# Kernel tuning notes

Hardware: AMD Instinct MI355X
Metric: run time of the kernel (lower is better)

Reference implementation:

```python
import jax, jax.numpy as jnp
import numpy as np

B, S, LQ = 32, 1024, 128
EMB = 256; H = 256; NH = 8; DH = H // NH
NCATE, NCONT, NNODE = 4, 8, 4
VOCAB = 50000
EPS = 1e-5
LK = S - LQ


def _ln(x, g, b):
    mu = jnp.mean(x, -1, keepdims=True)
    xc = x - mu
    var = jnp.mean(xc * xc, -1, keepdims=True)
    return xc * jax.lax.rsqrt(var + EPS) * g + b


def _leaky(x):
    return jnp.where(x >= 0, x, 0.01 * x)  # LeakyReLU slope 0.01 (torch default)


def setup_inputs() -> dict:
    key = jax.random.key(0)
    ks = jax.random.split(key, 48)
    rnd = lambda i, shape, scale=0.02: jax.random.normal(ks[i], shape, dtype=jnp.float32) * scale
    rng = np.random.default_rng(0)
    qidx = jnp.asarray(np.sort(rng.choice(S, LQ, replace=False)).astype(np.int64))
    cate_table = rnd(6, (VOCAB, EMB)).at[0].set(0.0)  # padding_idx=0
    inp = {
        "node": jax.random.normal(ks[0], (B, S, EMB * NNODE), dtype=jnp.float32),
        "cate": jax.random.randint(ks[1], (B, S, NCATE), 0, VOCAB),
        "cont": jax.random.normal(ks[2], (B, S, NCONT), dtype=jnp.float32),
        "query_index": qidx,
        "mask": jax.random.bernoulli(ks[3], 0.1, (B, LK)),
        "cate_table": cate_table,
        "pos_emb": rnd(4, (1, S, H)),
        "node_W": rnd(5, (EMB * NNODE, H)), "node_b": jnp.zeros((H,), jnp.float32),
        "node_ln_g": jnp.ones((H,), jnp.float32), "node_ln_b": jnp.zeros((H,), jnp.float32),
        "cate_W": rnd(7, (EMB * NCATE, H)), "cate_b": jnp.zeros((H,), jnp.float32),
        "cate_ln_g": jnp.ones((H,), jnp.float32), "cate_ln_b": jnp.zeros((H,), jnp.float32),
        "bn_g": jnp.ones((NCONT,), jnp.float32), "bn_b": jnp.zeros((NCONT,), jnp.float32),
        "cont_W": rnd(8, (NCONT, H)), "cont_b": jnp.zeros((H,), jnp.float32),
        "cont_ln_g": jnp.ones((H,), jnp.float32), "cont_ln_b": jnp.zeros((H,), jnp.float32),
        "comb_W": rnd(9, (3 * H, H)), "comb_b": jnp.zeros((H,), jnp.float32),
        "comb_ln_g": jnp.ones((H,), jnp.float32), "comb_ln_b": jnp.zeros((H,), jnp.float32),
        "q_W": rnd(10, (H, H)), "q_b": jnp.zeros((H,), jnp.float32),
        "k_W": rnd(11, (H, H)), "k_b": jnp.zeros((H,), jnp.float32),
        "v_W": rnd(12, (H, H)), "v_b": jnp.zeros((H,), jnp.float32),
        "reg_W1": rnd(13, (H, H)), "reg_b1": jnp.zeros((H,), jnp.float32),
        "reg_ln_g": jnp.ones((H,), jnp.float32), "reg_ln_b": jnp.zeros((H,), jnp.float32),
        "reg_W2": rnd(14, (H, H)), "reg_b2": jnp.zeros((H,), jnp.float32),
    }
    return inp


def reference(node, cate, cont, query_index, mask, cate_table, pos_emb,
              node_W, node_b, node_ln_g, node_ln_b,
              cate_W, cate_b, cate_ln_g, cate_ln_b,
              bn_g, bn_b, cont_W, cont_b, cont_ln_g, cont_ln_b,
              comb_W, comb_b, comb_ln_g, comb_ln_b,
              q_W, q_b, k_W, k_b, v_W, v_b,
              reg_W1, reg_b1, reg_ln_g, reg_ln_b, reg_W2, reg_b2):
    # --- three embedding branches: Linear -> LayerNorm ---
    node_e = _ln(node @ node_W + node_b, node_ln_g, node_ln_b)
    ce = cate_table[cate].reshape(B, S, NCATE * EMB)  # embedding gather
    cate_e = _ln(ce @ cate_W + cate_b, cate_ln_g, cate_ln_b)
    # BatchNorm1d (training-mode batch stats, biased var) over flattened [B*S, C]
    cf = cont.reshape(-1, NCONT)
    mu = jnp.mean(cf, 0)
    var = jnp.mean((cf - mu) ** 2, 0)
    cn = ((cf - mu) * jax.lax.rsqrt(var + EPS) * bn_g + bn_b).reshape(B, S, NCONT)
    cont_e = _ln(cn @ cont_W + cont_b, cont_ln_g, cont_ln_b)
    # --- combine + positions ---
    seq = jnp.concatenate([node_e, cate_e, cont_e], -1)       # [B,S,3H]
    seq = _ln(_leaky(seq) @ comb_W + comb_b, comb_ln_g, comb_ln_b) + pos_emb  # [B,S,H]
    # --- gather-split cross attention: queries vs complement keys ---
    is_q = jnp.zeros((S,), bool).at[query_index].set(True)
    key_index = jnp.nonzero(~is_q, size=LK)[0]                # setdiff1d, static size
    q = seq[:, query_index]                                   # [B,LQ,H]
    kv = seq[:, key_index]                                    # [B,LK,H]
    Q = (q @ q_W + q_b).reshape(B, LQ, NH, DH).transpose(0, 2, 1, 3)
    K = (kv @ k_W + k_b).reshape(B, LK, NH, DH).transpose(0, 2, 1, 3)
    V = (kv @ v_W + v_b).reshape(B, LK, NH, DH).transpose(0, 2, 1, 3)
    scale = jnp.float32(1.0 / np.sqrt(DH))
    scores = jnp.einsum('bhqd,bhkd->bhqk', Q, K) * scale      # [B,NH,LQ,LK]
    scores = jnp.where(mask[:, None, None, :], jnp.float32(-1e9), scores)
    attn = jax.nn.softmax(scores, -1)                         # dropout = identity (eval)
    out = jnp.einsum('bhqk,bhkd->bhqd', attn, V).transpose(0, 2, 1, 3).reshape(B, LQ, H)
    h = _leaky(_ln(out @ reg_W1 + reg_b1, reg_ln_g, reg_ln_b))
    return h @ reg_W2 + reg_b2                                # [B,LQ,H]
```

## Files before the change

kernel.cpp:

```cpp
#include <hip/hip_runtime.h>
#include <cstdint>

#define EPSV 1e-5f
#define AS1 __attribute__((address_space(1)))
#define AS3 __attribute__((address_space(3)))

#define VMCNT_BAR(N) do { \
    asm volatile("s_waitcnt vmcnt(" #N ") lgkmcnt(0)" ::: "memory"); \
    __builtin_amdgcn_sched_barrier(0); \
    __builtin_amdgcn_s_barrier(); } while (0)

typedef __attribute__((ext_vector_type(8))) short short8v;
typedef __attribute__((ext_vector_type(4))) float float4v;

__device__ inline unsigned short f2bf(float f) {
    union { float f; unsigned int u; } v; v.f = f;
    unsigned int r = v.u + 0x7FFF + ((v.u >> 16) & 1);
    return (unsigned short)(r >> 16);
}

__device__ inline size_t bidx(int n, int k) {
    return ((size_t)(k >> 5) << 13) + ((size_t)(n >> 4) << 9)
         + (((k >> 3) & 3) << 7) + ((n & 15) << 3) + (k & 7);
}

__device__ inline void gld16(const unsigned short* g, unsigned short* d) {
    __builtin_amdgcn_global_load_lds((const AS1 void*)g, (AS3 void*)d, 16, 0, 0);
}

__device__ inline void issue_b(const unsigned short* Bc, int s, unsigned short* bsb,
                               int w, int l) {
    const unsigned short* g = Bc + ((size_t)s << 13) + (w << 9) + (l << 3);
    unsigned short* d = bsb + (w << 9) + (l << 3);
    #pragma unroll
    for (int i = 0; i < 4; ++i)
        gld16(g + (i << 11), d + (i << 11));
}

__global__ __launch_bounds__(256) void wt_all_k(
    const float* __restrict__ nW, const float* __restrict__ cW, const float* __restrict__ mW,
    const float* __restrict__ qW, const float* __restrict__ kW, const float* __restrict__ vW,
    const float* __restrict__ r1W, const float* __restrict__ r2W,
    unsigned short* __restrict__ nO, unsigned short* __restrict__ cO, unsigned short* __restrict__ mO,
    unsigned short* __restrict__ qO, unsigned short* __restrict__ kO, unsigned short* __restrict__ vO,
    unsigned short* __restrict__ r1O, unsigned short* __restrict__ r2O)
{
    __shared__ float T[64][65];
    int bid = blockIdx.x;
    const float* W; unsigned short* O; int K, tile;
    if (bid < 64)       { W = nW; O = nO; K = 1024; tile = bid; }
    else if (bid < 128) { W = cW; O = cO; K = 1024; tile = bid - 64; }
    else if (bid < 176) { W = mW; O = mO; K = 768;  tile = bid - 128; }
    else {
        int s = (bid - 176) >> 4; tile = (bid - 176) & 15; K = 256;
        switch (s) {
            case 0: W = qW;  O = qO;  break;
            case 1: W = kW;  O = kO;  break;
            case 2: W = vW;  O = vO;  break;
            case 3: W = r1W; O = r1O; break;
            default: W = r2W; O = r2O; break;
        }
    }
    int kTiles = K >> 6;
    int k0 = (tile % kTiles) * 64, n0 = (tile / kTiles) * 64;
    int c = threadIdx.x & 63, r4 = threadIdx.x >> 6;
    #pragma unroll
    for (int rr = 0; rr < 64; rr += 4) {
        int r = rr + r4;
        T[r][c] = W[(size_t)(k0 + r) * 256 + n0 + c];
    }
    __syncthreads();
    #pragma unroll
    for (int rr = 0; rr < 64; rr += 4) {
        int n = rr + r4;
        O[bidx(n0 + n, k0 + c)] = f2bf(T[c][n]);
    }
}

__global__ __launch_bounds__(256) void gemm_nc_k(
    const float* __restrict__ node, const int* __restrict__ cate,
    const float* __restrict__ table,
    const unsigned short* __restrict__ nWt, const unsigned short* __restrict__ cWt,
    const float* __restrict__ nb, const float* __restrict__ cb,
    const float* __restrict__ nlg, const float* __restrict__ nlb,
    const float* __restrict__ clg, const float* __restrict__ clb,
    unsigned short* __restrict__ Y)
{
    __shared__ union UN {
        unsigned short A[2][4096];
        struct { float S[64][4]; float Q[64][4]; } red;
    } U;
    __shared__ unsigned short Bs[2][16384];
    const int t = threadIdx.x;
    const bool isC = blockIdx.x >= 512;
    const int bm = (isC ? (int)blockIdx.x - 512 : (int)blockIdx.x) * 64;
    const int w = t >> 6, l = t & 63, lr = l & 15, lg = l >> 4;
    const int ar = t >> 2;
    const int ac = (t & 3) * 16;
    const int aw0 = (((t & 3) >> 1) << 11) + ((ar >> 4) << 9)
                  + ((((t & 3) * 2) & 3) << 7) + ((ar & 15) << 3);
    const int aw1 = aw0 + 128;

    const unsigned short* Bc = isC ? cWt : nWt;
    const float* bias = isC ? cb : nb;
    const float* lng  = isC ? clg : nlg;
    const float* lnbp = isC ? clb : nlb;
    const int colOff = isC ? 256 : 0;

    const float* apf = node + (size_t)(bm + ar) * 1024 + ac;
    int4 idx4 = {0,0,0,0};
    if (isC) idx4 = *(const int4*)&cate[(bm + ar) * 4];

    float4v acc[4][4];
    #pragma unroll
    for (int i = 0; i < 4; ++i)
        #pragma unroll
        for (int j = 0; j < 4; ++j) acc[i][j] = (float4v)0.f;

    float4 rA[4];

    auto loadA = [&](int s, float4 (&r)[4]) {
        const float* p;
        if (isC) {
            int kt = s * 64 + ac;
            int g = kt >> 8;
            int idx = (g == 0) ? idx4.x : (g == 1) ? idx4.y : (g == 2) ? idx4.z : idx4.w;
            p = table + (size_t)idx * 256 + (kt & 255);
        } else {
            p = apf + s * 64;
        }
        #pragma unroll
        for (int i = 0; i < 4; ++i) r[i] = *(const float4*)(p + i * 4);
    };
    auto writeA = [&](const float4 (&r)[4], unsigned short* Ab) {
        short8v v0, v1;
        v0[0] = (short)f2bf(r[0].x); v0[1] = (short)f2bf(r[0].y);
        v0[2] = (short)f2bf(r[0].z); v0[3] = (short)f2bf(r[0].w);
        v0[4] = (short)f2bf(r[1].x); v0[5] = (short)f2bf(r[1].y);
        v0[6] = (short)f2bf(r[1].z); v0[7] = (short)f2bf(r[1].w);
        v1[0] = (short)f2bf(r[2].x); v1[1] = (short)f2bf(r[2].y);
        v1[2] = (short)f2bf(r[2].z); v1[3] = (short)f2bf(r[2].w);
        v1[4] = (short)f2bf(r[3].x); v1[5] = (short)f2bf(r[3].y);
        v1[6] = (short)f2bf(r[3].z); v1[7] = (short)f2bf(r[3].w);
        *(short8v*)&Ab[aw0] = v0;
        *(short8v*)&Ab[aw1] = v1;
    };
    auto comp = [&](const unsigned short* Ab, const unsigned short* bsb) {
        #pragma unroll
        for (int kk = 0; kk < 2; ++kk) {
            short8v af[4], bf[4];
            #pragma unroll
            for (int i = 0; i < 4; ++i)
                af[i] = *(const short8v*)&Ab[kk*2048 + i*512 + lg*128 + lr*8];
            #pragma unroll
            for (int j = 0; j < 4; ++j)
                bf[j] = *(const short8v*)&bsb[kk*8192 + ((w*4 + j) << 9) + (lg << 7) + (lr << 3)];
            #pragma unroll
            for (int i = 0; i < 4; ++i)
                #pragma unroll
                for (int j = 0; j < 4; ++j)
                    acc[i][j] = __builtin_amdgcn_mfma_f32_16x16x32_bf16(af[i], bf[j], acc[i][j], 0, 0, 0);
        }
    };

    issue_b(Bc, 0, &Bs[0][0], w, l);
    issue_b(Bc, 1, &Bs[0][8192], w, l);
    loadA(0, rA);
    writeA(rA, U.A[0]);
    loadA(1, rA);
    asm volatile("s_waitcnt lgkmcnt(0)" ::: "memory");
    __builtin_amdgcn_sched_barrier(0);
    __builtin_amdgcn_s_barrier();

    for (int s = 0; s < 16; ++s) {
        const int cur = s & 1;
        if (s + 1 < 16) {
            issue_b(Bc, 2*(s+1),     &Bs[1 - cur][0],    w, l);
            issue_b(Bc, 2*(s+1) + 1, &Bs[1 - cur][8192], w, l);
        }
        comp(U.A[cur], &Bs[cur][0]);
        if (s + 1 < 16) {
            writeA(rA, U.A[1 - cur]);
            if (s + 2 < 16) {
                loadA(s + 2, rA);
                VMCNT_BAR(4);
            } else {
                VMCNT_BAR(0);
            }
        }
    }

    #pragma unroll
    for (int j = 0; j < 4; ++j) {
        float bvj = bias[w*64 + j*16 + lr];
        #pragma unroll
        for (int i = 0; i < 4; ++i)
            #pragma unroll
            for (int r4 = 0; r4 < 4; ++r4) acc[i][j][r4] += bvj;
    }
    __syncthreads();
    #pragma unroll
    for (int i = 0; i < 4; ++i) {
        float ps[4], qs[4];
        #pragma unroll
        for (int r4 = 0; r4 < 4; ++r4) {
            float a0 = acc[i][0][r4], a1 = acc[i][1][r4],
                  a2 = acc[i][2][r4], a3 = acc[i][3][r4];
            ps[r4] = (a0 + a1) + (a2 + a3);
            qs[r4] = (a0*a0 + a1*a1) + (a2*a2 + a3*a3);
        }
        #pragma unroll
        for (int o = 1; o < 16; o <<= 1)
            #pragma unroll
            for (int r4 = 0; r4 < 4; ++r4) {
                ps[r4] += __shfl_xor(ps[r4], o);
                qs[r4] += __shfl_xor(qs[r4], o);
            }
        if (lr == 0) {
            #pragma unroll
            for (int r4 = 0; r4 < 4; ++r4) {
                U.red.S[i*16 + lg*4 + r4][w] = ps[r4];
                U.red.Q[i*16 + lg*4 + r4][w] = qs[r4];
            }
        }
    }
    __syncthreads();
    #pragma unroll
    for (int i = 0; i < 4; ++i) {
        float mu[4], rstd[4];
        #pragma unroll
        for (int r4 = 0; r4 < 4; ++r4) {
            int rl = i*16 + lg*4 + r4;
            float s  = (U.red.S[rl][0] + U.red.S[rl][1]) + (U.red.S[rl][2] + U.red.S[rl][3]);
            float qq = (U.red.Q[rl][0] + U.red.Q[rl][1]) + (U.red.Q[rl][2] + U.red.Q[rl][3]);
            float m_ = s * (1.0f/256.0f);
            mu[r4] = m_;
            rstd[r4] = rsqrtf(qq * (1.0f/256.0f) - m_*m_ + EPSV);
        }
        #pragma unroll
        for (int j = 0; j < 4; ++j) {
            int c = w*64 + j*16 + lr;
            float gv = lng[c], b2 = lnbp[c];
            #pragma unroll
            for (int r4 = 0; r4 < 4; ++r4) {
                int row = bm + i*16 + lg*4 + r4;
                float y = (acc[i][j][r4] - mu[r4]) * rstd[r4] * gv + b2;
                y = (y >= 0.f) ? y : 0.01f*y;
                Y[(size_t)row * 768 + colOff + c] = f2bf(y);
            }
        }
    }
}

__global__ __launch_bounds__(256) void gemm_comb_k(
    const unsigned short* __restrict__ A,
    const unsigned short* __restrict__ Bc,
    const float* __restrict__ bias,
    const float* __restrict__ lng, const float* __restrict__ lnbp,
    const float* __restrict__ pos,
    unsigned short* __restrict__ Y)
{
    __shared__ union UC {
        unsigned short A[2][2048];
        struct { float S[32][4]; float Q[32][4]; } red;
    } U;
    __shared__ unsigned short Bs[2][16384];
    const int t = threadIdx.x;
    const int bm = blockIdx.x * 32;
    const int w = t >> 6, l = t & 63, lr = l & 15, lg = l >> 4;
    const int arow = t >> 3;
    const int ake  = (t & 7) * 8;
    const int awo = (((t & 7) >> 2) << 10) + ((arow >> 4) << 9)
                  + (((t & 7) & 3) << 7) + ((arow & 15) << 3);

    const unsigned short* ap = A + (size_t)(bm + arow) * 768 + ake;

    float4v acc[2][4];
    #pragma unroll
    for (int i = 0; i < 2; ++i)
        #pragma unroll
        for (int j = 0; j < 4; ++j) acc[i][j] = (float4v)0.f;

    short8v aA;

    auto comp = [&](const unsigned short* Ab, const unsigned short* bsb) {
        #pragma unroll
        for (int kk = 0; kk < 2; ++kk) {
            short8v af[2], bf[4];
            #pragma unroll
            for (int i = 0; i < 2; ++i)
                af[i] = *(const short8v*)&Ab[kk*1024 + i*512 + lg*128 + lr*8];
            #pragma unroll
            for (int j = 0; j < 4; ++j)
                bf[j] = *(const short8v*)&bsb[kk*8192 + ((w*4 + j) << 9) + (lg << 7) + (lr << 3)];
            #pragma unroll
            for (int i = 0; i < 2; ++i)
                #pragma unroll
                for (int j = 0; j < 4; ++j)
                    acc[i][j] = __builtin_amdgcn_mfma_f32_16x16x32_bf16(af[i], bf[j], acc[i][j], 0, 0, 0);
        }
    };

    issue_b(Bc, 0, &Bs[0][0], w, l);
    issue_b(Bc, 1, &Bs[0][8192], w, l);
    aA = *(const short8v*)(ap);
    *(short8v*)&U.A[0][awo] = aA;
    aA = *(const short8v*)(ap + 64);
    asm volatile("s_waitcnt lgkmcnt(0)" ::: "memory");
    __builtin_amdgcn_sched_barrier(0);
    __builtin_amdgcn_s_barrier();

    for (int s = 0; s < 12; ++s) {
        const int cur = s & 1;
        if (s + 1 < 12) {
            issue_b(Bc, 2*(s+1),     &Bs[1 - cur][0],    w, l);
            issue_b(Bc, 2*(s+1) + 1, &Bs[1 - cur][8192], w, l);
        }
        comp(U.A[cur], &Bs[cur][0]);
        if (s + 1 < 12) {
            *(short8v*)&U.A[1 - cur][awo] = aA;
            if (s + 2 < 12) {
                aA = *(const short8v*)(ap + (s + 2) * 64);
                VMCNT_BAR(1);
            } else {
                VMCNT_BAR(0);
            }
        }
    }

    #pragma unroll
    for (int j = 0; j < 4; ++j) {
        float bvj = bias[w*64 + j*16 + lr];
        #pragma unroll
        for (int i = 0; i < 2; ++i)
            #pragma unroll
            for (int r4 = 0; r4 < 4; ++r4) acc[i][j][r4] += bvj;
    }
    __syncthreads();
    #pragma unroll
    for (int i = 0; i < 2; ++i) {
        float ps[4], qs[4];
        #pragma unroll
        for (int r4 = 0; r4 < 4; ++r4) {
            float a0 = acc[i][0][r4], a1 = acc[i][1][r4],
                  a2 = acc[i][2][r4], a3 = acc[i][3][r4];
            ps[r4] = (a0 + a1) + (a2 + a3);
            qs[r4] = (a0*a0 + a1*a1) + (a2*a2 + a3*a3);
        }
        #pragma unroll
        for (int o = 1; o < 16; o <<= 1)
            #pragma unroll
            for (int r4 = 0; r4 < 4; ++r4) {
                ps[r4] += __shfl_xor(ps[r4], o);
                qs[r4] += __shfl_xor(qs[r4], o);
            }
        if (lr == 0) {
            #pragma unroll
            for (int r4 = 0; r4 < 4; ++r4) {
                U.red.S[i*16 + lg*4 + r4][w] = ps[r4];
                U.red.Q[i*16 + lg*4 + r4][w] = qs[r4];
            }
        }
    }
    __syncthreads();
    #pragma unroll
    for (int i = 0; i < 2; ++i) {
        float mu[4], rstd[4];
        #pragma unroll
        for (int r4 = 0; r4 < 4; ++r4) {
            int rl = i*16 + lg*4 + r4;
            float s  = (U.red.S[rl][0] + U.red.S[rl][1]) + (U.red.S[rl][2] + U.red.S[rl][3]);
            float qq = (U.red.Q[rl][0] + U.red.Q[rl][1]) + (U.red.Q[rl][2] + U.red.Q[rl][3]);
            float m_ = s * (1.0f/256.0f);
            mu[r4] = m_;
            rstd[r4] = rsqrtf(qq * (1.0f/256.0f) - m_*m_ + EPSV);
        }
        #pragma unroll
        for (int j = 0; j < 4; ++j) {
            int c = w*64 + j*16 + lr;
            float gv = lng[c], b2 = lnbp[c];
            #pragma unroll
            for (int r4 = 0; r4 < 4; ++r4) {
                int row = bm + i*16 + lg*4 + r4;
                float y = (acc[i][j][r4] - mu[r4]) * rstd[r4] * gv + b2
                        + pos[(size_t)(row & 1023) * 256 + c];
                Y[(size_t)row * 256 + c] = f2bf(y);
            }
        }
    }
}

__global__ __launch_bounds__(256) void gemm_qkv_k(
    const unsigned short* __restrict__ seq,
    const int* __restrict__ qmap, const int* __restrict__ krmap,
    const unsigned short* __restrict__ qWt, const unsigned short* __restrict__ kWt,
    const unsigned short* __restrict__ vWt,
    const float* __restrict__ qb, const float* __restrict__ kb, const float* __restrict__ vb,
    unsigned short* __restrict__ Qo, unsigned short* __restrict__ Ko,
    unsigned short* __restrict__ Vt)
{
    __shared__ unsigned short Asl[2][4096];
    __shared__ unsigned short Bs[2][16384];
    const int t = threadIdx.x;
    const int bid = blockIdx.x;
    int seg, bm;
    const int* gmap; const unsigned short* Bc; const float* bias;
    if (bid < 64)       { seg = 0; bm = bid * 64;         gmap = qmap;  Bc = qWt; bias = qb; }
    else if (bid < 512) { seg = 1; bm = (bid - 64) * 64;  gmap = krmap; Bc = kWt; bias = kb; }
    else                { seg = 2; bm = (bid - 512) * 64; gmap = krmap; Bc = vWt; bias = vb; }
    const int w = t >> 6, l = t & 63, lr = l & 15, lg = l >> 4;
    const int ar = t >> 2;
    const int ac = (t & 3) * 16;
    const int aw0 = (((t & 3) >> 1) << 11) + ((ar >> 4) << 9)
                  + ((((t & 3) * 2) & 3) << 7) + ((ar & 15) << 3);
    const int aw1 = aw0 + 128;

    const unsigned short* ap = seq + (size_t)gmap[bm + ar] * 256 + ac;

    float4v acc[4][4];
    #pragma unroll
    for (int i = 0; i < 4; ++i)
        #pragma unroll
        for (int j = 0; j < 4; ++j) acc[i][j] = (float4v)0.f;

    short8v a0A, a1A;

    auto comp = [&](const unsigned short* Ab, const unsigned short* bsb) {
        #pragma unroll
        for (int kk = 0; kk < 2; ++kk) {
            short8v af[4], bf[4];
            #pragma unroll
            for (int i = 0; i < 4; ++i)
                af[i] = *(const short8v*)&Ab[kk*2048 + i*512 + lg*128 + lr*8];
            #pragma unroll
            for (int j = 0; j < 4; ++j)
                bf[j] = *(const short8v*)&bsb[kk*8192 + ((w*4 + j) << 9) + (lg << 7) + (lr << 3)];
            #pragma unroll
            for (int i = 0; i < 4; ++i)
                #pragma unroll
                for (int j = 0; j < 4; ++j)
                    acc[i][j] = __builtin_amdgcn_mfma_f32_16x16x32_bf16(af[i], bf[j], acc[i][j], 0, 0, 0);
        }
    };

    issue_b(Bc, 0, &Bs[0][0], w, l);
    issue_b(Bc, 1, &Bs[0][8192], w, l);
    a0A = *(const short8v*)(ap);
    a1A = *(const short8v*)(ap + 8);
    *(short8v*)&Asl[0][aw0] = a0A;
    *(short8v*)&Asl[0][aw1] = a1A;
    a0A = *(const short8v*)(ap + 64);
    a1A = *(const short8v*)(ap + 72);
    asm volatile("s_waitcnt lgkmcnt(0)" ::: "memory");
    __builtin_amdgcn_sched_barrier(0);
    __builtin_amdgcn_s_barrier();

    for (int s = 0; s < 4; ++s) {
        const int cur = s & 1;
        if (s + 1 < 4) {
            issue_b(Bc, 2*(s+1),     &Bs[1 - cur][0],    w, l);
            issue_b(Bc, 2*(s+1) + 1, &Bs[1 - cur][8192], w, l);
        }
        comp(Asl[cur], &Bs[cur][0]);
        if (s + 1 < 4) {
            *(short8v*)&Asl[1 - cur][aw0] = a0A;
            *(short8v*)&Asl[1 - cur][aw1] = a1A;
            if (s + 2 < 4) {
                a0A = *(const short8v*)(ap + (s + 2) * 64);
                a1A = *(const short8v*)(ap + (s + 2) * 64 + 8);
                VMCNT_BAR(2);
            } else {
                VMCNT_BAR(0);
            }
        }
    }

    unsigned short* outp = (seg == 0) ? Qo : (seg == 1) ? Ko : Vt;
    #pragma unroll
    for (int j = 0; j < 4; ++j) {
        int c = w*64 + j*16 + lr;
        float bvj = bias[c];
        #pragma unroll
        for (int i = 0; i < 4; ++i) {
            #pragma unroll
            for (int r4 = 0; r4 < 4; ++r4) {
                int rl = i*16 + lg*4 + r4;
                float val = acc[i][j][r4] + bvj;
                if (seg < 2) {
                    outp[(size_t)(bm + rl) * 256 + c] = f2bf(val);
                } else {
                    int vbk = bm / 896;
                    int kl = bm - vbk * 896 + rl;
                    outp[((size_t)vbk * 256 + c) * 896 + kl] = f2bf(val);
                }
            }
        }
    }
}

template<int EPI>
__global__ __launch_bounds__(256) void gemm_reg_k(
    const unsigned short* __restrict__ Asrc,
    const unsigned short* __restrict__ Bc,
    const float* __restrict__ bias,
    const float* __restrict__ ln_g,
    const float* __restrict__ ln_b,
    void* __restrict__ Cout)
{
    __shared__ union UR {
        unsigned short A[2][4096];
        struct { float S[64][4]; float Q[64][4]; } red;
    } U;
    __shared__ unsigned short Bs[2][16384];
    const int t = threadIdx.x;
    const int bm = blockIdx.x * 64;
    const int w = t >> 6, l = t & 63, lr = l & 15, lg = l >> 4;
    const int ar = t >> 2;
    const int ac = (t & 3) * 16;
    const int aw0 = (((t & 3) >> 1) << 11) + ((ar >> 4) << 9)
                  + ((((t & 3) * 2) & 3) << 7) + ((ar & 15) << 3);
    const int aw1 = aw0 + 128;

    const unsigned short* ap = Asrc + (size_t)(bm + ar) * 256 + ac;

    float4v acc[4][4];
    #pragma unroll
    for (int i = 0; i < 4; ++i)
        #pragma unroll
        for (int j = 0; j < 4; ++j) acc[i][j] = (float4v)0.f;

    short8v a0A, a1A, a0B, a1B;

    auto comp = [&](const unsigned short* Ab, const unsigned short* bsb) {
        #pragma unroll
        for (int kk = 0; kk < 2; ++kk) {
            short8v af[4], bf[4];
            #pragma unroll
            for (int i = 0; i < 4; ++i)
                af[i] = *(const short8v*)&Ab[kk*2048 + i*512 + lg*128 + lr*8];
            #pragma unroll
            for (int j = 0; j < 4; ++j)
                bf[j] = *(const short8v*)&bsb[kk*8192 + ((w*4 + j) << 9) + (lg << 7) + (lr << 3)];
            #pragma unroll
            for (int i = 0; i < 4; ++i)
                #pragma unroll
                for (int j = 0; j < 4; ++j)
                    acc[i][j] = __builtin_amdgcn_mfma_f32_16x16x32_bf16(af[i], bf[j], acc[i][j], 0, 0, 0);
        }
    };

    issue_b(Bc, 0, &Bs[0][0], w, l);
    issue_b(Bc, 1, &Bs[0][8192], w, l);
    a0A = *(const short8v*)(ap);
    a1A = *(const short8v*)(ap + 8);
    for (int s = 0; s < 4; ++s) {
        int cur = s & 1;
        __syncthreads();
        *(short8v*)&U.A[cur][aw0] = a0A;
        *(short8v*)&U.A[cur][aw1] = a1A;
        __syncthreads();
        if (s + 1 < 4) {
            issue_b(Bc, 2*(s+1),     &Bs[1 - cur][0],    w, l);
            issue_b(Bc, 2*(s+1) + 1, &Bs[1 - cur][8192], w, l);
            a0B = *(const short8v*)(ap + (s + 1) * 64);
            a1B = *(const short8v*)(ap + (s + 1) * 64 + 8);
        }
        comp(U.A[cur], &Bs[cur][0]);
        a0A = a0B; a1A = a1B;
    }

    #pragma unroll
    for (int j = 0; j < 4; ++j) {
        float bvj = bias[w*64 + j*16 + lr];
        #pragma unroll
        for (int i = 0; i < 4; ++i)
            #pragma unroll
            for (int r4 = 0; r4 < 4; ++r4) acc[i][j][r4] += bvj;
    }

    if (EPI == 0) {
        #pragma unroll
        for (int i = 0; i < 4; ++i)
            #pragma unroll
            for (int j = 0; j < 4; ++j) {
                int c = w*64 + j*16 + lr;
                #pragma unroll
                for (int r4 = 0; r4 < 4; ++r4) {
                    int rl = i*16 + lg*4 + r4;
                    ((float*)Cout)[(size_t)(bm + rl) * 256 + c] = acc[i][j][r4];
                }
            }
    } else {
        __syncthreads();
        #pragma unroll
        for (int i = 0; i < 4; ++i) {
            float ps[4], qs[4];
            #pragma unroll
            for (int r4 = 0; r4 < 4; ++r4) {
                float a0 = acc[i][0][r4], a1 = acc[i][1][r4],
                      a2 = acc[i][2][r4], a3 = acc[i][3][r4];
                ps[r4] = (a0 + a1) + (a2 + a3);
                qs[r4] = (a0*a0 + a1*a1) + (a2*a2 + a3*a3);
            }
            #pragma unroll
            for (int o = 1; o < 16; o <<= 1)
                #pragma unroll
                for (int r4 = 0; r4 < 4; ++r4) {
                    ps[r4] += __shfl_xor(ps[r4], o);
                    qs[r4] += __shfl_xor(qs[r4], o);
                }
            if (lr == 0) {
                #pragma unroll
                for (int r4 = 0; r4 < 4; ++r4) {
                    U.red.S[i*16 + lg*4 + r4][w] = ps[r4];
                    U.red.Q[i*16 + lg*4 + r4][w] = qs[r4];
                }
            }
        }
        __syncthreads();
        #pragma unroll
        for (int i = 0; i < 4; ++i) {
            float mu[4], rstd[4];
            #pragma unroll
            for (int r4 = 0; r4 < 4; ++r4) {
                int rl = i*16 + lg*4 + r4;
                float s  = (U.red.S[rl][0] + U.red.S[rl][1]) + (U.red.S[rl][2] + U.red.S[rl][3]);
                float qq = (U.red.Q[rl][0] + U.red.Q[rl][1]) + (U.red.Q[rl][2] + U.red.Q[rl][3]);
                float m_ = s * (1.0f/256.0f);
                mu[r4] = m_;
                rstd[r4] = rsqrtf(qq * (1.0f/256.0f) - m_*m_ + EPSV);
            }
            #pragma unroll
            for (int j = 0; j < 4; ++j) {
                int c = w*64 + j*16 + lr;
                float gv = ln_g[c], b2 = ln_b[c];
                #pragma unroll
                for (int r4 = 0; r4 < 4; ++r4) {
                    int row = bm + i*16 + lg*4 + r4;
                    float y = (acc[i][j][r4] - mu[r4]) * rstd[r4] * gv + b2;
                    y = (y >= 0.f) ? y : 0.01f*y;
                    ((unsigned short*)Cout)[(size_t)row * 256 + c] = f2bf(y);
                }
            }
        }
    }
}

__global__ __launch_bounds__(256) void bn_stats_k(const float* __restrict__ cont,
                                                  float* __restrict__ stats)
{
    __shared__ float ss[8], sq[8];
    int tid = threadIdx.x;
    if (tid < 8) { ss[tid] = 0.f; sq[tid] = 0.f; }
    __syncthreads();
    int gt = blockIdx.x * 256 + tid;
    float s = 0.f, q = 0.f;
    for (int e = gt; e < 32768*8; e += 256*256) { float v = cont[e]; s += v; q += v*v; }
    int f = gt & 7;
    atomicAdd(&ss[f], s);
    atomicAdd(&sq[f], q);
    __syncthreads();
    if (tid < 8) { atomicAdd(&stats[tid], ss[tid]); atomicAdd(&stats[8+tid], sq[tid]); }
}

__global__ __launch_bounds__(256) void cont_k(
    const float* __restrict__ cont, const float* __restrict__ stats,
    const float* __restrict__ bn_g, const float* __restrict__ bn_b,
    const float* __restrict__ W, const float* __restrict__ bias,
    const float* __restrict__ g, const float* __restrict__ bL,
    unsigned short* __restrict__ seq3)
{
    __shared__ float Ws[8][256];
    __shared__ float sscale[8], sshift[8];
    __shared__ float cr[8];
    __shared__ float red[8];
    int tid = threadIdx.x;
    #pragma unroll
    for (int d = 0; d < 8; ++d) Ws[d][tid] = W[d*256 + tid];
    if (tid < 8) {
        float mean = stats[tid] * (1.0f/32768.0f);
        float var  = stats[8+tid] * (1.0f/32768.0f) - mean*mean;
        float r = rsqrtf(var + EPSV);
        float sc = r * bn_g[tid];
        sscale[tid] = sc;
        sshift[tid] = bn_b[tid] - mean*sc;
    }
    __syncthreads();
    int lane = tid & 63, wv = tid >> 6;
    float gv = g[tid], bv = bL[tid], biasv = bias[tid];
    for (int row = blockIdx.x; row < 32768; row += gridDim.x) {
        if (tid < 8) cr[tid] = cont[(size_t)row*8 + tid]*sscale[tid] + sshift[tid];
        __syncthreads();
        float acc = biasv;
        #pragma unroll
        for (int d = 0; d < 8; ++d) acc += cr[d]*Ws[d][tid];
        float s = acc;
        #pragma unroll
        for (int o = 32; o; o >>= 1) s += __shfl_xor(s, o);
        if (lane == 0) red[wv] = s;
        __syncthreads();
        float mu = (red[0]+red[1]+red[2]+red[3]) * (1.0f/256.0f);
        float dc = acc - mu;
        float qv = dc*dc;
        #pragma unroll
        for (int o = 32; o; o >>= 1) qv += __shfl_xor(qv, o);
        if (lane == 0) red[4+wv] = qv;
        __syncthreads();
        float var = (red[4]+red[5]+red[6]+red[7]) * (1.0f/256.0f);
        float y = dc * rsqrtf(var + EPSV) * gv + bv;
        y = (y >= 0.f) ? y : 0.01f*y;
        seq3[(size_t)row*768 + 512 + tid] = f2bf(y);
        __syncthreads();
    }
}

__global__ void build_maps_k(const int* __restrict__ qidx, int* __restrict__ kmap)
{
    __shared__ int flag[1024];
    __shared__ int scan[1024];
    int t = threadIdx.x;
    flag[t] = 0;
    __syncthreads();
    if (t < 128) flag[qidx[t]] = 1;
    __syncthreads();
    int nq = 1 - flag[t];
    scan[t] = nq;
    __syncthreads();
    for (int off = 1; off < 1024; off <<= 1) {
        int v = (t >= off) ? scan[t - off] : 0;
        __syncthreads();
        scan[t] += v;
        __syncthreads();
    }
    if (nq) kmap[scan[t] - 1] = t;
}

__global__ void expand_maps_k(const int* __restrict__ qidx, const int* __restrict__ kmap,
                              int* __restrict__ qmap, int* __restrict__ krmap)
{
    int i = blockIdx.x * 256 + threadIdx.x;
    if (i < 32*128) { int b = i >> 7; int t = i & 127; qmap[i] = b*1024 + qidx[t]; }
    if (i < 32*896) { int b = i / 896; int t = i - b*896; krmap[i] = b*1024 + kmap[t]; }
}

__global__ __launch_bounds__(256) void mask_sniff_k(const unsigned char* __restrict__ msrc,
                                                    int* __restrict__ flags)
{
    int i = blockIdx.x * 256 + threadIdx.x;
    unsigned char v = msrc[i];
    bool u8  = v && (i & 3);
    bool i32 = v && !(i & 3) && ((i & 7) == 4);
    unsigned long long bu = __ballot(u8);
    unsigned long long bi = __ballot(i32);
    if ((threadIdx.x & 63) == 0) {
        if (bu) atomicOr(&flags[0], 1);
        if (bi) atomicOr(&flags[1], 1);
    }
}

__global__ __launch_bounds__(256) void mask_conv_k(const unsigned char* __restrict__ msrc,
                                                   const int* __restrict__ flags,
                                                   unsigned char* __restrict__ mu8)
{
    int i = blockIdx.x * 256 + threadIdx.x;
    int mode = flags[0] ? 0 : (flags[1] ? 1 : 2);
    unsigned char v;
    if (mode == 0)      v = msrc[i] ? 1 : 0;
    else if (mode == 1) v = ((const int*)msrc)[i] ? 1 : 0;
    else                v = ((const long long*)msrc)[i] ? 1 : 0;
    mu8[i] = v;
}

__global__ __launch_bounds__(256) void attn_mfma_k(
    const unsigned short* __restrict__ Qb,
    const unsigned short* __restrict__ Kb,
    const unsigned short* __restrict__ Vtb,
    const unsigned char* __restrict__ mask,
    unsigned short* __restrict__ out)
{
    __shared__ unsigned short Pw[4][16][72];
    const int t = threadIdx.x;
    const int w = t >> 6, l = t & 63;
    const int lr = l & 15, lg = l >> 4;
    const int bx = blockIdx.x;
    const int qh = bx & 1, h = (bx >> 1) & 7, b = bx >> 4;
    const int qrow0 = b*128 + qh*64 + w*16;

    short8v qf = *(const short8v*)&Qb[(size_t)(qrow0 + lr)*256 + h*32 + lg*8];

    const unsigned short* Kbase = Kb + (size_t)b*896*256 + h*32;
    const unsigned short* Vbase = Vtb + ((size_t)b*256 + h*32)*896;
    const unsigned char* mrow = mask + b*896;

    float4v O0 = (float4v)0.f, O1 = (float4v)0.f;
    float m[4], lsum[4];
    #pragma unroll
    for (int r = 0; r < 4; ++r) { m[r] = -3.0e38f; lsum[r] = 0.f; }

    short8v kf[4], vf[4];
    int mk[4];
    #pragma unroll
    for (int i = 0; i < 4; ++i) {
        kf[i] = *(const short8v*)&Kbase[(size_t)(i*16 + lr)*256 + lg*8];
        mk[i] = mrow[i*16 + lr];
    }
    #pragma unroll
    for (int kc = 0; kc < 2; ++kc)
        #pragma unroll
        for (int nt = 0; nt < 2; ++nt)
            vf[kc*2+nt] = *(const short8v*)&Vbase[(size_t)(nt*16 + lr)*896 + kc*32 + lg*8];

    for (int kt3 = 0; kt3 < 14; ++kt3) {
        const int kb2 = kt3*64 + 64;
        short8v kf2[4], vf2[4];
        int mk2[4];
        if (kt3 < 13) {
            #pragma unroll
            for (int i = 0; i < 4; ++i) {
                kf2[i] = *(const short8v*)&Kbase[(size_t)(kb2 + i*16 + lr)*256 + lg*8];
                mk2[i] = mrow[kb2 + i*16 + lr];
            }
            #pragma unroll
            for (int kc = 0; kc < 2; ++kc)
                #pragma unroll
                for (int nt = 0; nt < 2; ++nt)
                    vf2[kc*2+nt] = *(const short8v*)&Vbase[(size_t)(nt*16 + lr)*896 + kb2 + kc*32 + lg*8];
        }
        float4v s4[4];
        #pragma unroll
        for (int i = 0; i < 4; ++i)
            s4[i] = __builtin_amdgcn_mfma_f32_16x16x32_bf16(qf, kf[i], (float4v)0.f, 0, 0, 0);
        #pragma unroll
        for (int i = 0; i < 4; ++i)
            #pragma unroll
            for (int r = 0; r < 4; ++r)
                s4[i][r] = mk[i] ? -1e9f : s4[i][r] * 0.17677669529663687f;
        float tm[4];
        #pragma unroll
        for (int r = 0; r < 4; ++r)
            tm[r] = fmaxf(fmaxf(s4[0][r], s4[1][r]), fmaxf(s4[2][r], s4[3][r]));
        #pragma unroll
        for (int o = 1; o < 16; o <<= 1)
            #pragma unroll
            for (int r = 0; r < 4; ++r) tm[r] = fmaxf(tm[r], __shfl_xor(tm[r], o));
        float resc[4];
        #pragma unroll
        for (int r = 0; r < 4; ++r) {
            float mn = fmaxf(m[r], tm[r]);
            resc[r] = __expf(m[r] - mn);
            m[r] = mn;
        }
        float rs[4] = {0.f, 0.f, 0.f, 0.f};
        #pragma unroll
        for (int i = 0; i < 4; ++i)
            #pragma unroll
            for (int r = 0; r < 4; ++r) {
                float p = __expf(s4[i][r] - m[r]);
                s4[i][r] = p;
                rs[r] += p;
            }
        #pragma unroll
        for (int o = 1; o < 16; o <<= 1)
            #pragma unroll
            for (int r = 0; r < 4; ++r) rs[r] += __shfl_xor(rs[r], o);
        #pragma unroll
        for (int r = 0; r < 4; ++r) lsum[r] = lsum[r]*resc[r] + rs[r];
        #pragma unroll
        for (int r = 0; r < 4; ++r) { O0[r] *= resc[r]; O1[r] *= resc[r]; }
        #pragma unroll
        for (int i = 0; i < 4; ++i)
            #pragma unroll
            for (int r = 0; r < 4; ++r)
                Pw[w][lg*4 + r][i*16 + lr] = f2bf(s4[i][r]);
        #pragma unroll
        for (int kc = 0; kc < 2; ++kc) {
            short8v pf = *(const short8v*)&Pw[w][lr][kc*32 + lg*8];
            O0 = __builtin_amdgcn_mfma_f32_16x16x32_bf16(pf, vf[kc*2+0], O0, 0, 0, 0);
            O1 = __builtin_amdgcn_mfma_f32_16x16x32_bf16(pf, vf[kc*2+1], O1, 0, 0, 0);
        }
        if (kt3 < 13) {
            #pragma unroll
            for (int i = 0; i < 4; ++i) { kf[i] = kf2[i]; mk[i] = mk2[i]; vf[i] = vf2[i]; }
        }
    }
    #pragma unroll
    for (int r = 0; r < 4; ++r) {
        float inv = 1.0f / lsum[r];
        size_t row = (size_t)(qrow0 + lg*4 + r);
        out[row*256 + h*32 + lr]      = f2bf(O0[r] * inv);
        out[row*256 + h*32 + 16 + lr] = f2bf(O1[r] * inv);
    }
}

extern "C" void kernel_launch(void* const* d_in, const int* in_sizes, int n_in,
                              void* d_out, int out_size, void* d_ws, size_t ws_size,
                              hipStream_t stream)
{
    const float* node       = (const float*)d_in[0];
    const int*   cate       = (const int*)d_in[1];
    const float* cont       = (const float*)d_in[2];
    const int*   qidx       = (const int*)d_in[3];
    const unsigned char* mask = (const unsigned char*)d_in[4];
    const float* cate_table = (const float*)d_in[5];
    const float* pos_emb    = (const float*)d_in[6];
    const float* node_W     = (const float*)d_in[7];
    const float* node_b     = (const float*)d_in[8];
    const float* node_ln_g  = (const float*)d_in[9];
    const float* node_ln_b  = (const float*)d_in[10];
    const float* cate_W     = (const float*)d_in[11];
    const float* cate_b     = (const float*)d_in[12];
    const float* cate_ln_g  = (const float*)d_in[13];
    const float* cate_ln_b  = (const float*)d_in[14];
    const float* bn_g       = (const float*)d_in[15];
    const float* bn_b       = (const float*)d_in[16];
    const float* cont_W     = (const float*)d_in[17];
    const float* cont_b     = (const float*)d_in[18];
    const float* cont_ln_g  = (const float*)d_in[19];
    const float* cont_ln_b  = (const float*)d_in[20];
    const float* comb_W     = (const float*)d_in[21];
    const float* comb_b     = (const float*)d_in[22];
    const float* comb_ln_g  = (const float*)d_in[23];
    const float* comb_ln_b  = (const float*)d_in[24];
    const float* q_W        = (const float*)d_in[25];
    const float* q_b        = (const float*)d_in[26];
    const float* k_W        = (const float*)d_in[27];
    const float* k_b        = (const float*)d_in[28];
    const float* v_W        = (const float*)d_in[29];
    const float* v_b        = (const float*)d_in[30];
    const float* reg_W1     = (const float*)d_in[31];
    const float* reg_b1     = (const float*)d_in[32];
    const float* reg_ln_g   = (const float*)d_in[33];
    const float* reg_ln_b   = (const float*)d_in[34];
    const float* reg_W2     = (const float*)d_in[35];
    const float* reg_b2     = (const float*)d_in[36];

    char* ws = (char*)d_ws;
    unsigned short* seq3bf = (unsigned short*)(ws + 0);
    unsigned short* seqbf  = (unsigned short*)(ws + 83886080);
    unsigned short* Qbf    = (unsigned short*)(ws + 100663296);
    unsigned short* Kbf    = (unsigned short*)(ws + 102760448);
    unsigned short* Vtbf   = (unsigned short*)(ws + 117440512);
    unsigned short* AObf   = (unsigned short*)(ws + 132120576);
    unsigned short* Hbf    = (unsigned short*)(ws + 0);
    float* stats = (float*)(ws + 165675008);
    int*   flags = (int*)  (ws + 165675072);
    int*   kmap  = (int*)  (ws + 165675136);
    int*   qmap  = (int*)  (ws + 165678720);
    int*   krmap = (int*)  (ws + 165695104);
    unsigned char* mu8 = (unsigned char*)(ws + 165809792);
    unsigned short* node_Wt = (unsigned short*)(ws + 165838464);
    unsigned short* cate_Wt = (unsigned short*)(ws + 166362752);
    unsigned short* comb_Wt = (unsigned short*)(ws + 166887040);
    unsigned short* q_Wt    = (unsigned short*)(ws + 167280256);
    unsigned short* k_Wt    = (unsigned short*)(ws + 167411328);
    unsigned short* v_Wt    = (unsigned short*)(ws + 167542400);
    unsigned short* r1_Wt   = (unsigned short*)(ws + 167673472);
    unsigned short* r2_Wt   = (unsigned short*)(ws + 167804544);
    float* outp = (float*)d_out;

    hipMemsetAsync(stats, 0, 128, stream);
    bn_stats_k<<<256, 256, 0, stream>>>(cont, stats);
    mask_sniff_k<<<112, 256, 0, stream>>>(mask, flags);
    mask_conv_k<<<112, 256, 0, stream>>>(mask, flags, mu8);
    wt_all_k<<<256, 256, 0, stream>>>(node_W, cate_W, comb_W, q_W, k_W, v_W, reg_W1, reg_W2,
                                      node_Wt, cate_Wt, comb_Wt, q_Wt, k_Wt, v_Wt, r1_Wt, r2_Wt);

    gemm_nc_k<<<1024, 256, 0, stream>>>(node, cate, cate_table, node_Wt, cate_Wt,
        node_b, cate_b, node_ln_g, node_ln_b, cate_ln_g, cate_ln_b, seq3bf);
    cont_k<<<2048, 256, 0, stream>>>(cont, stats, bn_g, bn_b, cont_W, cont_b,
                                     cont_ln_g, cont_ln_b, seq3bf);
    gemm_comb_k<<<1024, 256, 0, stream>>>(seq3bf, comb_Wt, comb_b,
        comb_ln_g, comb_ln_b, pos_emb, seqbf);
    build_maps_k<<<1, 1024, 0, stream>>>(qidx, kmap);
    expand_maps_k<<<112, 256, 0, stream>>>(qidx, kmap, qmap, krmap);
    gemm_qkv_k<<<960, 256, 0, stream>>>(seqbf, qmap, krmap, q_Wt, k_Wt, v_Wt,
        q_b, k_b, v_b, Qbf, Kbf, Vtbf);
    attn_mfma_k<<<512, 256, 0, stream>>>(Qbf, Kbf, Vtbf, mu8, AObf);
    gemm_reg_k<3><<<64, 256, 0, stream>>>(AObf, r1_Wt, reg_b1, reg_ln_g, reg_ln_b, Hbf);
    gemm_reg_k<0><<<64, 256, 0, stream>>>(Hbf, r2_Wt, reg_b2, nullptr, nullptr, outp);
}
```

Baseline: 269.4 us.

## Use 512-thread blocks with 2x4 wave split in node/cate and QKV GEMMs

The node/cate GEMM and the QKV projection GEMM now launch 512 threads per block instead of 256. Eight waves are arranged 2x4 over the 64x256 tile, so each wave holds half as many accumulators and loads half the A data per thread. B-tile loading is rewritten for eight waves. Pipeline waits are simplified to a full vmcnt(0) drain, including in the comb GEMM, which may reduce overlap of global loads with compute. The aim is more waves per CU and lower register pressure, to better hide latency.

```diff
diff --git a/kernel.cpp b/kernel.cpp
--- a/kernel.cpp
+++ b/kernel.cpp
@@ -35,6 +35,16 @@
     #pragma unroll
     for (int i = 0; i < 4; ++i)
         gld16(g + (i << 11), d + (i << 11));
+}
+
+__device__ inline void issue_b8(const unsigned short* Bc, int s, unsigned short* bsb,
+                                int w, int l) {
+    const unsigned short* g = Bc + ((size_t)(2 * s) << 13);
+    #pragma unroll
+    for (int i = 0; i < 4; ++i) {
+        int blk = (w + i * 8) << 9;
+        gld16(g + blk + (l << 3), bsb + blk + (l << 3));
+    }
 }
 
 __global__ __launch_bounds__(256) void wt_all_k(
@@ -77,7 +87,7 @@
     }
 }
 
-__global__ __launch_bounds__(256) void gemm_nc_k(
+__global__ __launch_bounds__(512, 4) void gemm_nc_k(
     const float* __restrict__ node, const int* __restrict__ cate,
     const float* __restrict__ table,
     const unsigned short* __restrict__ nWt, const unsigned short* __restrict__ cWt,
@@ -95,11 +105,11 @@
     const bool isC = blockIdx.x >= 512;
     const int bm = (isC ? (int)blockIdx.x - 512 : (int)blockIdx.x) * 64;
     const int w = t >> 6, l = t & 63, lr = l & 15, lg = l >> 4;
-    const int ar = t >> 2;
-    const int ac = (t & 3) * 16;
-    const int aw0 = (((t & 3) >> 1) << 11) + ((ar >> 4) << 9)
-                  + ((((t & 3) * 2) & 3) << 7) + ((ar & 15) << 3);
-    const int aw1 = aw0 + 128;
+    const int wm = w >> 2, wn = w & 3;
+    const int ar = t >> 3;
+    const int ac = (t & 7) * 8;
+    const int aw = ((ac >> 5) << 11) + ((ar >> 4) << 9)
+                 + (((ac >> 3) & 3) << 7) + ((ar & 15) << 3);
 
     const unsigned short* Bc = isC ? cWt : nWt;
     const float* bias = isC ? cb : nb;
@@ -111,15 +121,15 @@
     int4 idx4 = {0,0,0,0};
     if (isC) idx4 = *(const int4*)&cate[(bm + ar) * 4];
 
-    float4v acc[4][4];
-    #pragma unroll
-    for (int i = 0; i < 4; ++i)
+    float4v acc[2][4];
+    #pragma unroll
+    for (int i = 0; i < 2; ++i)
         #pragma unroll
         for (int j = 0; j < 4; ++j) acc[i][j] = (float4v)0.f;
 
-    float4 rA[4];
-
-    auto loadA = [&](int s, float4 (&r)[4]) {
+    float4 rA0, rA1;
+
+    auto loadA = [&](int s) {
         const float* p;
         if (isC) {
             int kt = s * 64 + ac;
@@ -129,78 +139,67 @@
         } else {
             p = apf + s * 64;
         }
-        #pragma unroll
-        for (int i = 0; i < 4; ++i) r[i] = *(const float4*)(p + i * 4);
+        rA0 = *(const float4*)p;
+        rA1 = *(const float4*)(p + 4);
     };
-    auto writeA = [&](const float4 (&r)[4], unsigned short* Ab) {
-        short8v v0, v1;
-        v0[0] = (short)f2bf(r[0].x); v0[1] = (short)f2bf(r[0].y);
-        v0[2] = (short)f2bf(r[0].z); v0[3] = (short)f2bf(r[0].w);
-        v0[4] = (short)f2bf(r[1].x); v0[5] = (short)f2bf(r[1].y);
-        v0[6] = (short)f2bf(r[1].z); v0[7] = (short)f2bf(r[1].w);
-        v1[0] = (short)f2bf(r[2].x); v1[1] = (short)f2bf(r[2].y);
-        v1[2] = (short)f2bf(r[2].z); v1[3] = (short)f2bf(r[2].w);
-        v1[4] = (short)f2bf(r[3].x); v1[5] = (short)f2bf(r[3].y);
-        v1[6] = (short)f2bf(r[3].z); v1[7] = (short)f2bf(r[3].w);
-        *(short8v*)&Ab[aw0] = v0;
-        *(short8v*)&Ab[aw1] = v1;
+    auto writeA = [&](unsigned short* Ab) {
+        short8v v;
+        v[0] = (short)f2bf(rA0.x); v[1] = (short)f2bf(rA0.y);
+        v[2] = (short)f2bf(rA0.z); v[3] = (short)f2bf(rA0.w);
+        v[4] = (short)f2bf(rA1.x); v[5] = (short)f2bf(rA1.y);
+        v[6] = (short)f2bf(rA1.z); v[7] = (short)f2bf(rA1.w);
+        *(short8v*)&Ab[aw] = v;
     };
     auto comp = [&](const unsigned short* Ab, const unsigned short* bsb) {
         #pragma unroll
         for (int kk = 0; kk < 2; ++kk) {
-            short8v af[4], bf[4];
-            #pragma unroll
-            for (int i = 0; i < 4; ++i)
-                af[i] = *(const short8v*)&Ab[kk*2048 + i*512 + lg*128 + lr*8];
+            short8v af[2], bf[4];
+            #pragma unroll
+            for (int i = 0; i < 2; ++i)
+                af[i] = *(const short8v*)&Ab[kk*2048 + ((wm*2 + i) << 9) + (lg << 7) + (lr << 3)];
             #pragma unroll
             for (int j = 0; j < 4; ++j)
-                bf[j] = *(const short8v*)&bsb[kk*8192 + ((w*4 + j) << 9) + (lg << 7) + (lr << 3)];
-            #pragma unroll
-            for (int i = 0; i < 4; ++i)
+                bf[j] = *(const short8v*)&bsb[kk*8192 + ((wn*4 + j) << 9) + (lg << 7) + (lr << 3)];
+            #pragma unroll
+            for (int i = 0; i < 2; ++i)
                 #pragma unroll
                 for (int j = 0; j < 4; ++j)
                     acc[i][j] = __builtin_amdgcn_mfma_f32_16x16x32_bf16(af[i], bf[j], acc[i][j], 0, 0, 0);
         }
     };
 
-    issue_b(Bc, 0, &Bs[0][0], w, l);
-    issue_b(Bc, 1, &Bs[0][8192], w, l);
-    loadA(0, rA);
-    writeA(rA, U.A[0]);
-    loadA(1, rA);
+    issue_b8(Bc, 0, &Bs[0][0], w, l);
+    loadA(0);
+    writeA(U.A[0]);
+    loadA(1);
     asm volatile("s_waitcnt lgkmcnt(0)" ::: "memory");
     __builtin_amdgcn_sched_barrier(0);
     __builtin_amdgcn_s_barrier();
 
     for (int s = 0; s < 16; ++s) {
         const int cur = s & 1;
-        if (s + 1 < 16) {
-            issue_b(Bc, 2*(s+1),     &Bs[1 - cur][0],    w, l);
-            issue_b(Bc, 2*(s+1) + 1, &Bs[1 - cur][8192], w, l);
-        }
+        if (s + 1 < 16)
+            issue_b8(Bc, s + 1, &Bs[1 - cur][0], w, l);
         comp(U.A[cur], &Bs[cur][0]);
         if (s + 1 < 16) {
-            writeA(rA, U.A[1 - cur]);
-            if (s + 2 < 16) {
-                loadA(s + 2, rA);
-                VMCNT_BAR(4);
-            } else {
-                VMCNT_BAR(0);
-            }
+            writeA(U.A[1 - cur]);
+            if (s + 2 < 16)
+                loadA(s + 2);
+            VMCNT_BAR(0);
         }
     }
 
     #pragma unroll
     for (int j = 0; j < 4; ++j) {
-        float bvj = bias[w*64 + j*16 + lr];
-        #pragma unroll
-        for (int i = 0; i < 4; ++i)
+        float bvj = bias[wn*64 + j*16 + lr];
+        #pragma unroll
+        for (int i = 0; i < 2; ++i)
             #pragma unroll
             for (int r4 = 0; r4 < 4; ++r4) acc[i][j][r4] += bvj;
     }
     __syncthreads();
     #pragma unroll
-    for (int i = 0; i < 4; ++i) {
+    for (int i = 0; i < 2; ++i) {
         float ps[4], qs[4];
         #pragma unroll
         for (int r4 = 0; r4 < 4; ++r4) {
@@ -219,31 +218,32 @@
         if (lr == 0) {
             #pragma unroll
             for (int r4 = 0; r4 < 4; ++r4) {
-                U.red.S[i*16 + lg*4 + r4][w] = ps[r4];
-                U.red.Q[i*16 + lg*4 + r4][w] = qs[r4];
-            }
-        }
-    }
-    __syncthreads();
-    #pragma unroll
-    for (int i = 0; i < 4; ++i) {
+                int rlc = wm*32 + i*16 + lg*4 + r4;
+                U.red.S[rlc][wn] = ps[r4];
+                U.red.Q[rlc][wn] = qs[r4];
+            }
+        }
+    }
+    __syncthreads();
+    #pragma unroll
+    for (int i = 0; i < 2; ++i) {
         float mu[4], rstd[4];
         #pragma unroll
         for (int r4 = 0; r4 < 4; ++r4) {
-            int rl = i*16 + lg*4 + r4;
-            float s  = (U.red.S[rl][0] + U.red.S[rl][1]) + (U.red.S[rl][2] + U.red.S[rl][3]);
-            float qq = (U.red.Q[rl][0] + U.red.Q[rl][1]) + (U.red.Q[rl][2] + U.red.Q[rl][3]);
+            int rlc = wm*32 + i*16 + lg*4 + r4;
+            float s  = (U.red.S[rlc][0] + U.red.S[rlc][1]) + (U.red.S[rlc][2] + U.red.S[rlc][3]);
+            float qq = (U.red.Q[rlc][0] + U.red.Q[rlc][1]) + (U.red.Q[rlc][2] + U.red.Q[rlc][3]);
             float m_ = s * (1.0f/256.0f);
             mu[r4] = m_;
             rstd[r4] = rsqrtf(qq * (1.0f/256.0f) - m_*m_ + EPSV);
         }
         #pragma unroll
         for (int j = 0; j < 4; ++j) {
-            int c = w*64 + j*16 + lr;
+            int c = wn*64 + j*16 + lr;
             float gv = lng[c], b2 = lnbp[c];
             #pragma unroll
             for (int r4 = 0; r4 < 4; ++r4) {
-                int row = bm + i*16 + lg*4 + r4;
+                int row = bm + wm*32 + i*16 + lg*4 + r4;
                 float y = (acc[i][j][r4] - mu[r4]) * rstd[r4] * gv + b2;
                 y = (y >= 0.f) ? y : 0.01f*y;
                 Y[(size_t)row * 768 + colOff + c] = f2bf(y);
@@ -319,12 +319,9 @@
         comp(U.A[cur], &Bs[cur][0]);
         if (s + 1 < 12) {
             *(short8v*)&U.A[1 - cur][awo] = aA;
-            if (s + 2 < 12) {
+            if (s + 2 < 12)
                 aA = *(const short8v*)(ap + (s + 2) * 64);
-                VMCNT_BAR(1);
-            } else {
-                VMCNT_BAR(0);
-            }
+            VMCNT_BAR(0);
         }
     }
 
@@ -390,7 +387,7 @@
     }
 }
 
-__global__ __launch_bounds__(256) void gemm_qkv_k(
+__global__ __launch_bounds__(512, 4) void gemm_qkv_k(
     const unsigned short* __restrict__ seq,
     const int* __restrict__ qmap, const int* __restrict__ krmap,
     const unsigned short* __restrict__ qWt, const unsigned short* __restrict__ kWt,
@@ -409,82 +406,71 @@
     else if (bid < 512) { seg = 1; bm = (bid - 64) * 64;  gmap = krmap; Bc = kWt; bias = kb; }
     else                { seg = 2; bm = (bid - 512) * 64; gmap = krmap; Bc = vWt; bias = vb; }
     const int w = t >> 6, l = t & 63, lr = l & 15, lg = l >> 4;
-    const int ar = t >> 2;
-    const int ac = (t & 3) * 16;
-    const int aw0 = (((t & 3) >> 1) << 11) + ((ar >> 4) << 9)
-                  + ((((t & 3) * 2) & 3) << 7) + ((ar & 15) << 3);
-    const int aw1 = aw0 + 128;
-
-    const unsigned short* ap = seq + (size_t)gmap[bm + ar] * 256 + ac;
-
-    float4v acc[4][4];
-    #pragma unroll
-    for (int i = 0; i < 4; ++i)
+    const int wm = w >> 2, wn = w & 3;
+    const int ar = t >> 3;
+    const int ak = (t & 7) * 8;
+    const int aw = ((ak >> 5) << 11) + ((ar >> 4) << 9)
+                 + (((ak >> 3) & 3) << 7) + ((ar & 15) << 3);
+
+    const unsigned short* ap = seq + (size_t)gmap[bm + ar] * 256 + ak;
+
+    float4v acc[2][4];
+    #pragma unroll
+    for (int i = 0; i < 2; ++i)
         #pragma unroll
         for (int j = 0; j < 4; ++j) acc[i][j] = (float4v)0.f;
 
-    short8v a0A, a1A;
+    short8v aA;
 
     auto comp = [&](const unsigned short* Ab, const unsigned short* bsb) {
         #pragma unroll
         for (int kk = 0; kk < 2; ++kk) {
-            short8v af[4], bf[4];
-            #pragma unroll
-            for (int i = 0; i < 4; ++i)
-                af[i] = *(const short8v*)&Ab[kk*2048 + i*512 + lg*128 + lr*8];
+            short8v af[2], bf[4];
+            #pragma unroll
+            for (int i = 0; i < 2; ++i)
+                af[i] = *(const short8v*)&Ab[kk*2048 + ((wm*2 + i) << 9) + (lg << 7) + (lr << 3)];
             #pragma unroll
             for (int j = 0; j < 4; ++j)
-                bf[j] = *(const short8v*)&bsb[kk*8192 + ((w*4 + j) << 9) + (lg << 7) + (lr << 3)];
-            #pragma unroll
-            for (int i = 0; i < 4; ++i)
+                bf[j] = *(const short8v*)&bsb[kk*8192 + ((wn*4 + j) << 9) + (lg << 7) + (lr << 3)];
+            #pragma unroll
+            for (int i = 0; i < 2; ++i)
                 #pragma unroll
                 for (int j = 0; j < 4; ++j)
                     acc[i][j] = __builtin_amdgcn_mfma_f32_16x16x32_bf16(af[i], bf[j], acc[i][j], 0, 0, 0);
         }
     };
 
-    issue_b(Bc, 0, &Bs[0][0], w, l);
-    issue_b(Bc, 1, &Bs[0][8192], w, l);
-    a0A = *(const short8v*)(ap);
-    a1A = *(const short8v*)(ap + 8);
-    *(short8v*)&Asl[0][aw0] = a0A;
-    *(short8v*)&Asl[0][aw1] = a1A;
-    a0A = *(const short8v*)(ap + 64);
-    a1A = *(const short8v*)(ap + 72);
+    issue_b8(Bc, 0, &Bs[0][0], w, l);
+    aA = *(const short8v*)(ap);
+    *(short8v*)&Asl[0][aw] = aA;
+    aA = *(const short8v*)(ap + 64);
     asm volatile("s_waitcnt lgkmcnt(0)" ::: "memory");
     __builtin_amdgcn_sched_barrier(0);
     __builtin_amdgcn_s_barrier();
 
     for (int s = 0; s < 4; ++s) {
         const int cur = s & 1;
-        if (s + 1 < 4) {
-            issue_b(Bc, 2*(s+1),     &Bs[1 - cur][0],    w, l);
-            issue_b(Bc, 2*(s+1) + 1, &Bs[1 - cur][8192], w, l);
-        }
+        if (s + 1 < 4)
+            issue_b8(Bc, s + 1, &Bs[1 - cur][0], w, l);
         comp(Asl[cur], &Bs[cur][0]);
         if (s + 1 < 4) {
-            *(short8v*)&Asl[1 - cur][aw0] = a0A;
-            *(short8v*)&Asl[1 - cur][aw1] = a1A;
-            if (s + 2 < 4) {
-                a0A = *(const short8v*)(ap + (s + 2) * 64);
-                a1A = *(const short8v*)(ap + (s + 2) * 64 + 8);
-                VMCNT_BAR(2);
-            } else {
-                VMCNT_BAR(0);
-            }
+            *(short8v*)&Asl[1 - cur][aw] = aA;
+            if (s + 2 < 4)
+                aA = *(const short8v*)(ap + (s + 2) * 64);
+            VMCNT_BAR(0);
         }
     }
 
     unsigned short* outp = (seg == 0) ? Qo : (seg == 1) ? Ko : Vt;
     #pragma unroll
     for (int j = 0; j < 4; ++j) {
-        int c = w*64 + j*16 + lr;
+        int c = wn*64 + j*16 + lr;
         float bvj = bias[c];
         #pragma unroll
-        for (int i = 0; i < 4; ++i) {
+        for (int i = 0; i < 2; ++i) {
             #pragma unroll
             for (int r4 = 0; r4 < 4; ++r4) {
-                int rl = i*16 + lg*4 + r4;
+                int rl = wm*32 + i*16 + lg*4 + r4;
                 float val = acc[i][j][r4] + bvj;
                 if (seg < 2) {
                     outp[(size_t)(bm + rl) * 256 + c] = f2bf(val);
@@ -965,7 +951,7 @@
     wt_all_k<<<256, 256, 0, stream>>>(node_W, cate_W, comb_W, q_W, k_W, v_W, reg_W1, reg_W2,
                                       node_Wt, cate_Wt, comb_Wt, q_Wt, k_Wt, v_Wt, r1_Wt, r2_Wt);
 
-    gemm_nc_k<<<1024, 256, 0, stream>>>(node, cate, cate_table, node_Wt, cate_Wt,
+    gemm_nc_k<<<1024, 512, 0, stream>>>(node, cate, cate_table, node_Wt, cate_Wt,
         node_b, cate_b, node_ln_g, node_ln_b, cate_ln_g, cate_ln_b, seq3bf);
     cont_k<<<2048, 256, 0, stream>>>(cont, stats, bn_g, bn_b, cont_W, cont_b,
                                      cont_ln_g, cont_ln_b, seq3bf);
@@ -973,7 +959,7 @@
         comb_ln_g, comb_ln_b, pos_emb, seqbf);
     build_maps_k<<<1, 1024, 0, stream>>>(qidx, kmap);
     expand_maps_k<<<112, 256, 0, stream>>>(qidx, kmap, qmap, krmap);
-    gemm_qkv_k<<<960, 256, 0, stream>>>(seqbf, qmap, krmap, q_Wt, k_Wt, v_Wt,
+    gemm_qkv_k<<<960, 512, 0, stream>>>(seqbf, qmap, krmap, q_Wt, k_Wt, v_Wt,
         q_b, k_b, v_b, Qbf, Kbf, Vtbf);
     attn_mfma_k<<<512, 256, 0, stream>>>(Qbf, Kbf, Vtbf, mu8, AObf);
     gemm_reg_k<3><<<64, 256, 0, stream>>>(AObf, r1_Wt, reg_b1, reg_ln_g, reg_ln_b, Hbf);
```

After: 266.4 us. No clear change (-1.1%).
